# Optimization experiments

Measured on AMD Instinct MI355X. Metric: run time of the kernel, lower is better.

Reference implementation:

```python
import jax, jax.numpy as jnp
import numpy as np

DIM = 1024        # BIGNET_DIM
GROUP = 16        # Linear4Bit group_size
LORA = 20         # lora_dim hardcoded in Block
NLAYERS = 18      # 6 blocks * 3 QLoRALinear
NBLOCKS = 6
BATCH = 8192
EPS = 1e-5


def setup_inputs() -> dict:
    key = jax.random.key(0)
    ks = jax.random.split(key, 6)
    x = jax.random.normal(ks[0], (BATCH, DIM), jnp.float32)
    # int4 quantized base weights in [-8, 7], stored as int32
    qw = jax.random.randint(ks[1], (NLAYERS, DIM, DIM), -8, 8, jnp.int32)
    # per-(out_row, input-group) dequant scales
    scales = jax.random.uniform(ks[2], (NLAYERS, DIM, DIM // GROUP), jnp.float32,
                                minval=0.005, maxval=0.02)
    bias = jax.random.normal(ks[3], (NLAYERS, DIM), jnp.float32) * 0.01
    # lora_a: kaiming-uniform-like scale; lora_b: small nonzero (zeros in torch init,
    # randomized here so the LoRA path is numerically exercised)
    lora_a = jax.random.normal(ks[4], (NLAYERS, LORA, DIM), jnp.float32) / np.sqrt(DIM)
    lora_b = jax.random.normal(ks[5], (NLAYERS, DIM, LORA), jnp.float32) * 0.01
    ln_w = jnp.ones((NBLOCKS - 1, DIM), jnp.float32)
    ln_b = jnp.zeros((NBLOCKS - 1, DIM), jnp.float32)
    return dict(x=x, qw=qw, scales=scales, bias=bias,
                lora_a=lora_a, lora_b=lora_b, ln_w=ln_w, ln_b=ln_b)


def _qlora_linear(x, qw, sc, b, A, B):
    # dequantize: each group of 16 input cols of a row shares one scale
    w = (qw.astype(jnp.float32).reshape(DIM, DIM // GROUP, GROUP)
         * sc[:, :, None]).reshape(DIM, DIM)          # [out, in]
    base = x @ w.T + b                                # [N, out]
    lora = (x @ A.T) @ B.T                            # [N, r] @ [r, out]
    return base + lora


def _layernorm(x, w, b):
    m = jnp.mean(x, axis=-1, keepdims=True)
    v = jnp.mean((x - m) ** 2, axis=-1, keepdims=True)
    return (x - m) * jax.lax.rsqrt(v + EPS) * w + b


def reference(x, qw, scales, bias, lora_a, lora_b, ln_w, ln_b):
    h = x
    li = 0
    for blk in range(NBLOCKS):
        r = h
        for j in range(3):
            r = _qlora_linear(r, qw[li], scales[li], bias[li], lora_a[li], lora_b[li])
            if j < 2:
                r = jax.nn.relu(r)
            li += 1
        h = h + r  # residual
        if blk < NBLOCKS - 1:
            h = _layernorm(h, ln_w[blk], ln_b[blk])
    return h
```

## Files before the change

### kernel.cpp

```cpp
#include <hip/hip_runtime.h>
#include <cstdint>
#include <cstddef>

#define DIM      1024
#define GROUP    16
#define LORA     20
#define NLAYERS  18
#define NBLOCKS  6
#define BATCH    8192
#define EPS      1e-5f

typedef __bf16 bf16_8 __attribute__((ext_vector_type(8)));
typedef __bf16 bf16_4 __attribute__((ext_vector_type(4)));
typedef float  f32x4  __attribute__((ext_vector_type(4)));

__global__ __launch_bounds__(256, 3) void wprep_kernel(
    const int* __restrict__ qw, const float* __restrict__ sc,
    const float* __restrict__ la, const float* __restrict__ lb,
    __bf16* __restrict__ whi) {
  const int l  = blockIdx.x >> 7;
  const int og = (blockIdx.x >> 1) & 63;
  const int cg = blockIdx.x & 1;
  const int tid = threadIdx.x;
  const int tc = tid & 31;
  const int tr = tid >> 5;

  int4  q[2][2][2];
  float sv[2][2];
  size_t rowb[2];
#pragma unroll
  for (int u = 0; u < 2; ++u) {
    const int orow = og * 16 + tr * 2 + u;
    rowb[u] = ((size_t)l * DIM + orow) * DIM + cg * 512;
    const size_t scb = ((size_t)l * DIM + orow) * (DIM / GROUP) + cg * 32;
#pragma unroll
    for (int v = 0; v < 2; ++v) {
      const int c = v * 256 + tc * 8;
      q[u][v][0] = *(const int4*)&qw[rowb[u] + c];
      q[u][v][1] = *(const int4*)&qw[rowb[u] + c + 4];
      sv[u][v] = sc[scb + (c >> 4)];
    }
  }

  __shared__ __bf16 As[LORA * 512];
  __shared__ float  Bs[16 * LORA];

  const float* Abase = la + (size_t)l * LORA * DIM + cg * 512;
  const float* Bbase = lb + ((size_t)l * DIM + og * 16) * LORA;
  for (int i = tid; i < 16 * LORA; i += 256) Bs[i] = Bbase[i];
#pragma unroll
  for (int i = 0; i < 10; ++i) {
    const int f4 = i * 256 + tid;
    const float4 a = *(const float4*)(Abase + (size_t)(f4 >> 7) * DIM + (f4 & 127) * 4);
    const bf16_4 ab = {(__bf16)a.x, (__bf16)a.y, (__bf16)a.z, (__bf16)a.w};
    *(bf16_4*)&As[f4 * 4] = ab;
  }
  __syncthreads();

  float acc[2][16];
#pragma unroll
  for (int u = 0; u < 2; ++u)
#pragma unroll
    for (int v = 0; v < 2; ++v) {
      acc[u][v * 8 + 0] = q[u][v][0].x * sv[u][v];
      acc[u][v * 8 + 1] = q[u][v][0].y * sv[u][v];
      acc[u][v * 8 + 2] = q[u][v][0].z * sv[u][v];
      acc[u][v * 8 + 3] = q[u][v][0].w * sv[u][v];
      acc[u][v * 8 + 4] = q[u][v][1].x * sv[u][v];
      acc[u][v * 8 + 5] = q[u][v][1].y * sv[u][v];
      acc[u][v * 8 + 6] = q[u][v][1].z * sv[u][v];
      acc[u][v * 8 + 7] = q[u][v][1].w * sv[u][v];
    }

#pragma unroll 2
  for (int j = 0; j < LORA; ++j) {
    float af[2][8];
#pragma unroll
    for (int v = 0; v < 2; ++v) {
      const bf16_8 a8 = *(const bf16_8*)&As[j * 512 + v * 256 + tc * 8];
#pragma unroll
      for (int e = 0; e < 8; ++e) af[v][e] = (float)a8[e];
    }
#pragma unroll
    for (int u = 0; u < 2; ++u) {
      const float bj = Bs[(tr * 2 + u) * LORA + j];
#pragma unroll
      for (int v = 0; v < 2; ++v)
#pragma unroll
        for (int e = 0; e < 8; ++e) acc[u][v * 8 + e] += bj * af[v][e];
    }
  }

#pragma unroll
  for (int u = 0; u < 2; ++u) {
#pragma unroll
    for (int v = 0; v < 2; ++v) {
      bf16_8 hv;
#pragma unroll
      for (int e = 0; e < 8; ++e) hv[e] = (__bf16)acc[u][v * 8 + e];
      *(bf16_8*)&whi[rowb[u] + v * 256 + tc * 8] = hv;
    }
  }
}

__global__ __launch_bounds__(256) void xprep_kernel(
    const float* __restrict__ x, __bf16* __restrict__ hi) {
  const size_t i = (size_t)blockIdx.x * 256 + threadIdx.x;
  const float4 v = ((const float4*)x)[i];
  const bf16_4 hv = {(__bf16)v.x, (__bf16)v.y, (__bf16)v.z, (__bf16)v.w};
  ((bf16_4*)hi)[i] = hv;
}

#define GBUF    24576
#define GOFF_W  16384

__device__ __forceinline__ int swz_off(int row, int slot) {
  const int colb = (slot * 16) ^ ((row & 7) << 4);
  return (row * 128 + colb) >> 1;
}

template <int NISSUE>
__device__ __forceinline__ void stageR(const __bf16* __restrict__ g, int row0, int k0,
                                       __bf16* lds, int tid) {
#pragma unroll
  for (int i = 0; i < NISSUE; ++i) {
    const int D = i * 8192 + tid * 16;
    const int row = D >> 7;
    const int colb = (D & 127) ^ ((row & 7) << 4);
    const __bf16* gp = g + (size_t)(row0 + row) * DIM + k0 + (colb >> 1);
    __builtin_amdgcn_global_load_lds(
        (const __attribute__((address_space(1))) void*)gp,
        (__attribute__((address_space(3))) void*)(lds + i * 4096 + (tid >> 6) * 512), 16, 0, 0);
  }
}

template <int MODE>
__global__ __launch_bounds__(512, 1) void gemm1_kernel(
    const __bf16* __restrict__ X, const __bf16* __restrict__ Wh,
    const float* __restrict__ bias, __bf16* __restrict__ Oh,
    const float* __restrict__ Hin,
    const float2* __restrict__ stats,
    const float* __restrict__ lnw, const float* __restrict__ lnb,
    float* __restrict__ Sout) {
  __shared__ __bf16 smem[3 * GBUF];

  const int tid  = threadIdx.x;
  const int lane = tid & 63;
  const int wv   = tid >> 6;
  const int wm   = wv >> 2;
  const int wn2  = wv & 3;
  const int xcd = blockIdx.x & 7;
  const int kk2 = blockIdx.x >> 3;
  const int tm  = xcd * 4 + (kk2 >> 3);
  const int tn  = kk2 & 7;
  const int rowX = tm * 256, rowW = tn * 128;

  const int lr   = lane & 15;
  const int slot = lane >> 4;

  int offX[4], offW[4];
#pragma unroll
  for (int n = 0; n < 4; ++n) offX[n] = swz_off(wn2 * 64 + n * 16 + lr, slot);
#pragma unroll
  for (int m = 0; m < 4; ++m) offW[m] = GOFF_W + swz_off(wm * 64 + m * 16 + lr, slot);

  f32x4 acc[4][4];
#pragma unroll
  for (int m = 0; m < 4; ++m)
#pragma unroll
    for (int n = 0; n < 4; ++n) acc[m][n] = f32x4{0.f, 0.f, 0.f, 0.f};

  auto stage_tile = [&](int t) {
    __bf16* sb = smem + (t % 3) * GBUF;
    stageR<4>(X,  rowX, t * 64, sb, tid);
    stageR<2>(Wh, rowW, t * 64, sb + GOFF_W, tid);
  };

  auto compute_tile = [&](int t) {
    const __bf16* buf = smem + (t % 3) * GBUF;
#pragma unroll
    for (int kk = 0; kk < 2; ++kk) {
      const int kx = kk * 32;
      bf16_8 xf[4];
#pragma unroll
      for (int n = 0; n < 4; ++n) xf[n] = *(const bf16_8*)&buf[offX[n] ^ kx];
#pragma unroll
      for (int m = 0; m < 4; ++m) {
        const bf16_8 w_h = *(const bf16_8*)&buf[offW[m] ^ kx];
#pragma unroll
        for (int n = 0; n < 4; ++n)
          acc[m][n] = __builtin_amdgcn_mfma_f32_16x16x32_bf16(w_h, xf[n], acc[m][n], 0, 0, 0);
      }
    }
  };

  stage_tile(0); stage_tile(1);
  asm volatile("s_waitcnt vmcnt(6)" ::: "memory");
  __builtin_amdgcn_s_barrier();

#pragma unroll 1
  for (int kt = 0; kt < 14; ++kt) {
    stage_tile(kt + 2);
    compute_tile(kt);
    asm volatile("s_waitcnt vmcnt(6)" ::: "memory");
    __builtin_amdgcn_s_barrier();
  }
  compute_tile(14);
  asm volatile("s_waitcnt vmcnt(0)" ::: "memory");
  __builtin_amdgcn_s_barrier();
  compute_tile(15);

  const int g4 = slot * 4;
#pragma unroll
  for (int m = 0; m < 4; ++m) {
    const int feat = tn * 128 + wm * 64 + m * 16 + g4;
    const float4 bv = *(const float4*)&bias[feat];
    float4 wq, bq;
    if constexpr (MODE == 2) {
      wq = *(const float4*)&lnw[feat];
      bq = *(const float4*)&lnb[feat];
    }
#pragma unroll
    for (int n = 0; n < 4; ++n) {
      const int nb = tm * 256 + wn2 * 64 + n * 16 + lr;
      const size_t base = (size_t)nb * DIM + feat;
      float v0 = acc[m][n][0] + bv.x;
      float v1 = acc[m][n][1] + bv.y;
      float v2 = acc[m][n][2] + bv.z;
      float v3 = acc[m][n][3] + bv.w;
      if constexpr (MODE == 0) {
        const bf16_4 hv = {(__bf16)fmaxf(v0, 0.f), (__bf16)fmaxf(v1, 0.f),
                           (__bf16)fmaxf(v2, 0.f), (__bf16)fmaxf(v3, 0.f)};
        *(bf16_4*)&Oh[base] = hv;
      } else if constexpr (MODE == 1) {
        const float4 h = *(const float4*)&Hin[base];
        *(float4*)&Sout[base] = float4{v0 + h.x, v1 + h.y, v2 + h.z, v3 + h.w};
      } else {
        const float2 st = stats[nb];
        const float4 s = *(const float4*)&Hin[base];
        const float h0 = (s.x - st.x) * st.y * wq.x + bq.x;
        const float h1 = (s.y - st.x) * st.y * wq.y + bq.y;
        const float h2 = (s.z - st.x) * st.y * wq.z + bq.z;
        const float h3 = (s.w - st.x) * st.y * wq.w + bq.w;
        *(float4*)&Sout[base] = float4{v0 + h0, v1 + h1, v2 + h2, v3 + h3};
      }
    }
  }
}

__global__ __launch_bounds__(256) void normcast_kernel(
    const float* __restrict__ S, const float* __restrict__ w,
    const float* __restrict__ b, float2* __restrict__ stats,
    __bf16* __restrict__ phi) {
  const int row = blockIdx.x;
  const int tid = threadIdx.x;
  const int lane = tid & 63;
  const int wv = tid >> 6;
  const float4 v = ((const float4*)(S + (size_t)row * DIM))[tid];

  float s = v.x + v.y + v.z + v.w;
#pragma unroll
  for (int m = 32; m; m >>= 1) s += __shfl_xor(s, m, 64);
  __shared__ float red[8];
  if (lane == 0) red[wv] = s;
  __syncthreads();
  const float mean = (red[0] + red[1] + red[2] + red[3]) * (1.f / DIM);

  const float d0 = v.x - mean, d1 = v.y - mean, d2 = v.z - mean, d3 = v.w - mean;
  float q = d0 * d0 + d1 * d1 + d2 * d2 + d3 * d3;
#pragma unroll
  for (int m = 32; m; m >>= 1) q += __shfl_xor(q, m, 64);
  if (lane == 0) red[4 + wv] = q;
  __syncthreads();
  const float var = (red[4] + red[5] + red[6] + red[7]) * (1.f / DIM);
  const float inv = 1.f / sqrtf(var + EPS);

  if (tid == 0) stats[row] = float2{mean, inv};

  const float4 wv4 = ((const float4*)w)[tid];
  const float4 bv4 = ((const float4*)b)[tid];
  const bf16_4 hv = {(__bf16)(d0 * inv * wv4.x + bv4.x),
                     (__bf16)(d1 * inv * wv4.y + bv4.y),
                     (__bf16)(d2 * inv * wv4.z + bv4.z),
                     (__bf16)(d3 * inv * wv4.w + bv4.w)};
  ((bf16_4*)phi)[(size_t)row * (DIM / 4) + tid] = hv;
}

extern "C" void kernel_launch(void* const* d_in, const int* in_sizes, int n_in,
                              void* d_out, int out_size, void* d_ws, size_t ws_size,
                              hipStream_t stream) {
  const float* x   = (const float*)d_in[0];
  const int*   qw  = (const int*)d_in[1];
  const float* sc  = (const float*)d_in[2];
  const float* bias= (const float*)d_in[3];
  const float* la  = (const float*)d_in[4];
  const float* lb  = (const float*)d_in[5];
  const float* lnw = (const float*)d_in[6];
  const float* lnb = (const float*)d_in[7];
  float* out = (float*)d_out;
  char* ws = (char*)d_ws;

  __bf16* WHI = (__bf16*)(ws);
  __bf16* X0  = (__bf16*)(ws + 37748736);
  __bf16* X1  = (__bf16*)(ws + 54525952);
  float*  SA  = (float*)(ws + 71303168);
  float*  SB  = (float*)(ws + 104857600);
  float2* STT = (float2*)(ws + 138412032);
  (void)ws_size; (void)in_sizes; (void)n_in; (void)out_size;

  xprep_kernel<<<BATCH * DIM / (256 * 4), 256, 0, stream>>>(x, X0);
  wprep_kernel<<<NLAYERS * 128, 256, 0, stream>>>(qw, sc, la, lb, WHI);

  const dim3 ggrid(BATCH / 256 * (DIM / 128));
  for (int blk = 0; blk < NBLOCKS; ++blk) {
    const int li = blk * 3;
    const size_t w0 = (size_t)li * DIM * DIM;
    const size_t w1 = (size_t)(li + 1) * DIM * DIM;
    const size_t w2 = (size_t)(li + 2) * DIM * DIM;
    float* Scur = (blk & 1) ? SB : SA;
    float* Sprev = (blk & 1) ? SA : SB;

    gemm1_kernel<0><<<ggrid, 512, 0, stream>>>(
        X0, WHI + w0, bias + (size_t)li * DIM, X1,
        nullptr, nullptr, nullptr, nullptr, nullptr);
    gemm1_kernel<0><<<ggrid, 512, 0, stream>>>(
        X1, WHI + w1, bias + (size_t)(li + 1) * DIM, X0,
        nullptr, nullptr, nullptr, nullptr, nullptr);
    float* sout = (blk == NBLOCKS - 1) ? out : Scur;
    if (blk == 0) {
      gemm1_kernel<1><<<ggrid, 512, 0, stream>>>(
          X0, WHI + w2, bias + (size_t)(li + 2) * DIM, nullptr,
          x, nullptr, nullptr, nullptr, sout);
    } else {
      gemm1_kernel<2><<<ggrid, 512, 0, stream>>>(
          X0, WHI + w2, bias + (size_t)(li + 2) * DIM, nullptr,
          Sprev, STT, lnw + (size_t)(blk - 1) * DIM, lnb + (size_t)(blk - 1) * DIM,
          sout);
    }
    if (blk < NBLOCKS - 1) {
      normcast_kernel<<<BATCH, 256, 0, stream>>>(
          Scur, lnw + (size_t)blk * DIM, lnb + (size_t)blk * DIM, STT, X0);
    }
  }
}
```

Before: 525.1 us.

## Interleave global-to-LDS staging with MFMA phases using barriers and setprio

The main K loop of the GEMM is split into eight phases. Each phase issues one of the six global_load_lds stage loads for tile kt+2, does its LDS fragment reads, and then runs four MFMAs bracketed by barriers and s_setprio(1/0). The aim is to spread memory issue across the compute and to let waves alternate between memory and MFMA work in lockstep. In exchange it adds sixteen barriers per K iteration, which could cost more synchronization stall than it hides.

New measurement: 592.5 us. 1.13x slower.

```diff
diff --git a/kernel.cpp b/kernel.cpp
--- a/kernel.cpp
+++ b/kernel.cpp
@@ -119,21 +119,6 @@
   return (row * 128 + colb) >> 1;
 }
 
-template <int NISSUE>
-__device__ __forceinline__ void stageR(const __bf16* __restrict__ g, int row0, int k0,
-                                       __bf16* lds, int tid) {
-#pragma unroll
-  for (int i = 0; i < NISSUE; ++i) {
-    const int D = i * 8192 + tid * 16;
-    const int row = D >> 7;
-    const int colb = (D & 127) ^ ((row & 7) << 4);
-    const __bf16* gp = g + (size_t)(row0 + row) * DIM + k0 + (colb >> 1);
-    __builtin_amdgcn_global_load_lds(
-        (const __attribute__((address_space(1))) void*)gp,
-        (__attribute__((address_space(3))) void*)(lds + i * 4096 + (tid >> 6) * 512), 16, 0, 0);
-  }
-}
-
 template <int MODE>
 __global__ __launch_bounds__(512, 1) void gemm1_kernel(
     const __bf16* __restrict__ X, const __bf16* __restrict__ Wh,
@@ -170,10 +155,32 @@
 #pragma unroll
     for (int n = 0; n < 4; ++n) acc[m][n] = f32x4{0.f, 0.f, 0.f, 0.f};
 
+  auto stage_one = [&](int t, int idx) {
+    __bf16* sb = smem + (t % 3) * GBUF;
+    if (idx < 4) {
+      const int D = idx * 8192 + tid * 16;
+      const int row = D >> 7;
+      const int colb = (D & 127) ^ ((row & 7) << 4);
+      const __bf16* gp = X + (size_t)(rowX + row) * DIM + t * 64 + (colb >> 1);
+      __builtin_amdgcn_global_load_lds(
+          (const __attribute__((address_space(1))) void*)gp,
+          (__attribute__((address_space(3))) void*)(sb + idx * 4096 + (tid >> 6) * 512),
+          16, 0, 0);
+    } else {
+      const int i = idx - 4;
+      const int D = i * 8192 + tid * 16;
+      const int row = D >> 7;
+      const int colb = (D & 127) ^ ((row & 7) << 4);
+      const __bf16* gp = Wh + (size_t)(rowW + row) * DIM + t * 64 + (colb >> 1);
+      __builtin_amdgcn_global_load_lds(
+          (const __attribute__((address_space(1))) void*)gp,
+          (__attribute__((address_space(3))) void*)(sb + GOFF_W + i * 4096 + (tid >> 6) * 512),
+          16, 0, 0);
+    }
+  };
   auto stage_tile = [&](int t) {
-    __bf16* sb = smem + (t % 3) * GBUF;
-    stageR<4>(X,  rowX, t * 64, sb, tid);
-    stageR<2>(Wh, rowW, t * 64, sb + GOFF_W, tid);
+#pragma unroll
+    for (int idx = 0; idx < 6; ++idx) stage_one(t, idx);
   };
 
   auto compute_tile = [&](int t) {
@@ -200,10 +207,28 @@
 
 #pragma unroll 1
   for (int kt = 0; kt < 14; ++kt) {
-    stage_tile(kt + 2);
-    compute_tile(kt);
-    asm volatile("s_waitcnt vmcnt(6)" ::: "memory");
-    __builtin_amdgcn_s_barrier();
+    const __bf16* buf = smem + (kt % 3) * GBUF;
+    bf16_8 xf[4];
+#pragma unroll
+    for (int p = 0; p < 8; ++p) {
+      const int kk = p >> 2, m = p & 3;
+      const int kx = kk * 32;
+      if (p < 6) stage_one(kt + 2, p);
+      if (m == 0) {
+#pragma unroll
+        for (int n = 0; n < 4; ++n) xf[n] = *(const bf16_8*)&buf[offX[n] ^ kx];
+      }
+      const bf16_8 w_h = *(const bf16_8*)&buf[offW[m] ^ kx];
+      if (p == 7)
+        asm volatile("s_waitcnt vmcnt(6)" ::: "memory");
+      __builtin_amdgcn_s_barrier();
+      __builtin_amdgcn_s_setprio(1);
+#pragma unroll
+      for (int n = 0; n < 4; ++n)
+        acc[m][n] = __builtin_amdgcn_mfma_f32_16x16x32_bf16(w_h, xf[n], acc[m][n], 0, 0, 0);
+      __builtin_amdgcn_s_setprio(0);
+      __builtin_amdgcn_s_barrier();
+    }
   }
   compute_tile(14);
   asm volatile("s_waitcnt vmcnt(0)" ::: "memory");
```

## Fuse all GEMM and layernorm launches into one cooperative persistent kernel

Applied to the files above, without the earlier changes.

Replaces the 23 separate gemm and normcast launches with a single cooperative kernel of 256 workgroups that runs every phase in sequence, separated by grid-wide barriers. The layernorm/cast phase is rewritten so that each wave handles four rows with wave-level reductions only, and 256 blocks cover all 8192 rows. The aim is to remove per-launch overhead and tail gaps between kernels. In exchange it adds the cost of grid.sync, depends on every workgroup being co-resident on the 256 CUs, and moves the shared-memory array out of the former gemm1 kernel into the fused kernel.

New measurement: 1.228 ms. 2.34x slower.

```diff
diff --git a/kernel.cpp b/kernel.cpp
--- a/kernel.cpp
+++ b/kernel.cpp
@@ -1,6 +1,9 @@
 #include <hip/hip_runtime.h>
+#include <hip/hip_cooperative_groups.h>
 #include <cstdint>
 #include <cstddef>
+
+namespace cg = cooperative_groups;
 
 #define DIM      1024
 #define GROUP    16
@@ -20,7 +23,7 @@
     __bf16* __restrict__ whi) {
   const int l  = blockIdx.x >> 7;
   const int og = (blockIdx.x >> 1) & 63;
-  const int cg = blockIdx.x & 1;
+  const int cg_ = blockIdx.x & 1;
   const int tid = threadIdx.x;
   const int tc = tid & 31;
   const int tr = tid >> 5;
@@ -31,8 +34,8 @@
 #pragma unroll
   for (int u = 0; u < 2; ++u) {
     const int orow = og * 16 + tr * 2 + u;
-    rowb[u] = ((size_t)l * DIM + orow) * DIM + cg * 512;
-    const size_t scb = ((size_t)l * DIM + orow) * (DIM / GROUP) + cg * 32;
+    rowb[u] = ((size_t)l * DIM + orow) * DIM + cg_ * 512;
+    const size_t scb = ((size_t)l * DIM + orow) * (DIM / GROUP) + cg_ * 32;
 #pragma unroll
     for (int v = 0; v < 2; ++v) {
       const int c = v * 256 + tc * 8;
@@ -45,7 +48,7 @@
   __shared__ __bf16 As[LORA * 512];
   __shared__ float  Bs[16 * LORA];
 
-  const float* Abase = la + (size_t)l * LORA * DIM + cg * 512;
+  const float* Abase = la + (size_t)l * LORA * DIM + cg_ * 512;
   const float* Bbase = lb + ((size_t)l * DIM + og * 16) * LORA;
   for (int i = tid; i < 16 * LORA; i += 256) Bs[i] = Bbase[i];
 #pragma unroll
@@ -135,15 +138,12 @@
 }
 
 template <int MODE>
-__global__ __launch_bounds__(512, 1) void gemm1_kernel(
+__device__ __forceinline__ void gemm_phase(
     const __bf16* __restrict__ X, const __bf16* __restrict__ Wh,
     const float* __restrict__ bias, __bf16* __restrict__ Oh,
-    const float* __restrict__ Hin,
-    const float2* __restrict__ stats,
+    const float* __restrict__ Hin, const float2* __restrict__ stats,
     const float* __restrict__ lnw, const float* __restrict__ lnb,
-    float* __restrict__ Sout) {
-  __shared__ __bf16 smem[3 * GBUF];
-
+    float* __restrict__ Sout, __bf16* __restrict__ smem) {
   const int tid  = threadIdx.x;
   const int lane = tid & 63;
   const int wv   = tid >> 6;
@@ -248,42 +248,91 @@
   }
 }
 
-__global__ __launch_bounds__(256) void normcast_kernel(
+__device__ __forceinline__ void normcast_phase(
     const float* __restrict__ S, const float* __restrict__ w,
     const float* __restrict__ b, float2* __restrict__ stats,
     __bf16* __restrict__ phi) {
-  const int row = blockIdx.x;
   const int tid = threadIdx.x;
   const int lane = tid & 63;
   const int wv = tid >> 6;
-  const float4 v = ((const float4*)(S + (size_t)row * DIM))[tid];
-
-  float s = v.x + v.y + v.z + v.w;
-#pragma unroll
-  for (int m = 32; m; m >>= 1) s += __shfl_xor(s, m, 64);
-  __shared__ float red[8];
-  if (lane == 0) red[wv] = s;
-  __syncthreads();
-  const float mean = (red[0] + red[1] + red[2] + red[3]) * (1.f / DIM);
-
-  const float d0 = v.x - mean, d1 = v.y - mean, d2 = v.z - mean, d3 = v.w - mean;
-  float q = d0 * d0 + d1 * d1 + d2 * d2 + d3 * d3;
-#pragma unroll
-  for (int m = 32; m; m >>= 1) q += __shfl_xor(q, m, 64);
-  if (lane == 0) red[4 + wv] = q;
-  __syncthreads();
-  const float var = (red[4] + red[5] + red[6] + red[7]) * (1.f / DIM);
-  const float inv = 1.f / sqrtf(var + EPS);
-
-  if (tid == 0) stats[row] = float2{mean, inv};
-
-  const float4 wv4 = ((const float4*)w)[tid];
-  const float4 bv4 = ((const float4*)b)[tid];
-  const bf16_4 hv = {(__bf16)(d0 * inv * wv4.x + bv4.x),
-                     (__bf16)(d1 * inv * wv4.y + bv4.y),
-                     (__bf16)(d2 * inv * wv4.z + bv4.z),
-                     (__bf16)(d3 * inv * wv4.w + bv4.w)};
-  ((bf16_4*)phi)[(size_t)row * (DIM / 4) + tid] = hv;
+#pragma unroll 1
+  for (int rr = 0; rr < 4; ++rr) {
+    const int row = blockIdx.x * 32 + wv * 4 + rr;
+    const float* Sr = S + (size_t)row * DIM;
+    float4 v[4];
+#pragma unroll
+    for (int i = 0; i < 4; ++i) v[i] = ((const float4*)Sr)[i * 64 + lane];
+    float s = 0.f;
+#pragma unroll
+    for (int i = 0; i < 4; ++i) s += v[i].x + v[i].y + v[i].z + v[i].w;
+#pragma unroll
+    for (int m = 32; m; m >>= 1) s += __shfl_xor(s, m, 64);
+    const float mean = s * (1.f / DIM);
+    float q = 0.f;
+#pragma unroll
+    for (int i = 0; i < 4; ++i) {
+      const float d0 = v[i].x - mean, d1 = v[i].y - mean,
+                  d2 = v[i].z - mean, d3 = v[i].w - mean;
+      q += d0 * d0 + d1 * d1 + d2 * d2 + d3 * d3;
+    }
+#pragma unroll
+    for (int m = 32; m; m >>= 1) q += __shfl_xor(q, m, 64);
+    const float inv = 1.f / sqrtf(q * (1.f / DIM) + EPS);
+    if (lane == 0) stats[row] = float2{mean, inv};
+#pragma unroll
+    for (int i = 0; i < 4; ++i) {
+      const int f4 = i * 64 + lane;
+      const float4 wv4 = ((const float4*)w)[f4];
+      const float4 bv4 = ((const float4*)b)[f4];
+      const bf16_4 hv = {(__bf16)((v[i].x - mean) * inv * wv4.x + bv4.x),
+                         (__bf16)((v[i].y - mean) * inv * wv4.y + bv4.y),
+                         (__bf16)((v[i].z - mean) * inv * wv4.z + bv4.z),
+                         (__bf16)((v[i].w - mean) * inv * wv4.w + bv4.w)};
+      *(bf16_4*)&phi[(size_t)row * DIM + f4 * 4] = hv;
+    }
+  }
+}
+
+extern "C" __global__ void __launch_bounds__(512, 1) meganet_kernel(
+    const __bf16* __restrict__ WHI, const float* __restrict__ bias,
+    const float* __restrict__ lnw, const float* __restrict__ lnb,
+    const float* __restrict__ x, __bf16* __restrict__ X0,
+    __bf16* __restrict__ X1, float* __restrict__ SA, float* __restrict__ SB,
+    float2* __restrict__ STT, float* __restrict__ out) {
+  __shared__ __bf16 smem[3 * GBUF];
+  cg::grid_group grid = cg::this_grid();
+
+#pragma unroll 1
+  for (int blk = 0; blk < NBLOCKS; ++blk) {
+    const int li = blk * 3;
+    const size_t w0 = (size_t)li * DIM * DIM;
+    const size_t w1 = (size_t)(li + 1) * DIM * DIM;
+    const size_t w2 = (size_t)(li + 2) * DIM * DIM;
+    float* Scur = (blk & 1) ? SB : SA;
+    float* Sprev = (blk & 1) ? SA : SB;
+    float* sout = (blk == NBLOCKS - 1) ? out : Scur;
+
+    gemm_phase<0>(X0, WHI + w0, bias + (size_t)li * DIM, X1,
+                  nullptr, nullptr, nullptr, nullptr, nullptr, smem);
+    grid.sync();
+    gemm_phase<0>(X1, WHI + w1, bias + (size_t)(li + 1) * DIM, X0,
+                  nullptr, nullptr, nullptr, nullptr, nullptr, smem);
+    grid.sync();
+    if (blk == 0) {
+      gemm_phase<1>(X0, WHI + w2, bias + (size_t)(li + 2) * DIM, nullptr,
+                    x, nullptr, nullptr, nullptr, sout, smem);
+    } else {
+      gemm_phase<2>(X0, WHI + w2, bias + (size_t)(li + 2) * DIM, nullptr,
+                    Sprev, STT, lnw + (size_t)(blk - 1) * DIM,
+                    lnb + (size_t)(blk - 1) * DIM, sout, smem);
+    }
+    if (blk < NBLOCKS - 1) {
+      grid.sync();
+      normcast_phase(Scur, lnw + (size_t)blk * DIM, lnb + (size_t)blk * DIM,
+                     STT, X0);
+      grid.sync();
+    }
+  }
 }
 
 extern "C" void kernel_launch(void* const* d_in, const int* in_sizes, int n_in,
@@ -300,7 +349,8 @@
   float* out = (float*)d_out;
   char* ws = (char*)d_ws;
 
-  __bf16* WHI = (__bf16*)(ws);
+  const __bf16* WHI = (const __bf16*)(ws);
+  __bf16* WHIw = (__bf16*)(ws);
   __bf16* X0  = (__bf16*)(ws + 37748736);
   __bf16* X1  = (__bf16*)(ws + 54525952);
   float*  SA  = (float*)(ws + 71303168);
@@ -309,37 +359,11 @@
   (void)ws_size; (void)in_sizes; (void)n_in; (void)out_size;
 
   xprep_kernel<<<BATCH * DIM / (256 * 4), 256, 0, stream>>>(x, X0);
-  wprep_kernel<<<NLAYERS * 128, 256, 0, stream>>>(qw, sc, la, lb, WHI);
-
-  const dim3 ggrid(BATCH / 256 * (DIM / 128));
-  for (int blk = 0; blk < NBLOCKS; ++blk) {
-    const int li = blk * 3;
-    const size_t w0 = (size_t)li * DIM * DIM;
-    const size_t w1 = (size_t)(li + 1) * DIM * DIM;
-    const size_t w2 = (size_t)(li + 2) * DIM * DIM;
-    float* Scur = (blk & 1) ? SB : SA;
-    float* Sprev = (blk & 1) ? SA : SB;
-
-    gemm1_kernel<0><<<ggrid, 512, 0, stream>>>(
-        X0, WHI + w0, bias + (size_t)li * DIM, X1,
-        nullptr, nullptr, nullptr, nullptr, nullptr);
-    gemm1_kernel<0><<<ggrid, 512, 0, stream>>>(
-        X1, WHI + w1, bias + (size_t)(li + 1) * DIM, X0,
-        nullptr, nullptr, nullptr, nullptr, nullptr);
-    float* sout = (blk == NBLOCKS - 1) ? out : Scur;
-    if (blk == 0) {
-      gemm1_kernel<1><<<ggrid, 512, 0, stream>>>(
-          X0, WHI + w2, bias + (size_t)(li + 2) * DIM, nullptr,
-          x, nullptr, nullptr, nullptr, sout);
-    } else {
-      gemm1_kernel<2><<<ggrid, 512, 0, stream>>>(
-          X0, WHI + w2, bias + (size_t)(li + 2) * DIM, nullptr,
-          Sprev, STT, lnw + (size_t)(blk - 1) * DIM, lnb + (size_t)(blk - 1) * DIM,
-          sout);
-    }
-    if (blk < NBLOCKS - 1) {
-      normcast_kernel<<<BATCH, 256, 0, stream>>>(
-          Scur, lnw + (size_t)blk * DIM, lnb + (size_t)blk * DIM, STT, X0);
-    }
-  }
-}
+  wprep_kernel<<<NLAYERS * 128, 256, 0, stream>>>(qw, sc, la, lb, WHIw);
+
+  void* args[] = {(void*)&WHI, (void*)&bias, (void*)&lnw, (void*)&lnb,
+                  (void*)&x, (void*)&X0, (void*)&X1, (void*)&SA, (void*)&SB,
+                  (void*)&STT, (void*)&out};
+  hipLaunchCooperativeKernel((const void*)meganet_kernel, dim3(256), dim3(512),
+                             args, 0, stream);
+}
```
